# Kernel tuning notes

Hardware: AMD Instinct MI355X
Metric: run time of the kernel (lower is better)

The kernel has to match this reference:

```python
import jax, jax.numpy as jnp
import numpy as np
import math

N, E, D, H, L = 50000, 800000, 256, 8, 8
DK = D // H
DFF = 4 * D


def _layernorm(h, g, b, eps=1e-5):
    m = jnp.mean(h, axis=-1, keepdims=True)
    v = jnp.mean((h - m) ** 2, axis=-1, keepdims=True)
    return (h - m) * jax.lax.rsqrt(v + eps) * g + b


def setup_inputs() -> dict:
    key = jax.random.key(0)
    ks = jax.random.split(key, 16)
    s = 1.0 / math.sqrt(D)
    x = jax.random.normal(ks[0], (N, D), dtype=jnp.float32)
    # every node gets >=1 in-edge so z > 0 everywhere (as in real connected graphs)
    edge_src = jax.random.randint(ks[1], (E,), 0, N, dtype=jnp.int32)
    edge_dst = jnp.concatenate([
        jnp.arange(N, dtype=jnp.int32),
        jax.random.randint(ks[2], (E - N,), 0, N, dtype=jnp.int32),
    ])
    return {
        "x": x,
        "edge_src": edge_src,
        "edge_dst": edge_dst,
        "Wq": jax.random.normal(ks[3], (L, D, D), dtype=jnp.float32) * s,
        "bq": jnp.zeros((L, D), dtype=jnp.float32),
        "Wk": jax.random.normal(ks[4], (L, D, D), dtype=jnp.float32) * s,
        "Wv": jax.random.normal(ks[5], (L, D, D), dtype=jnp.float32) * s,
        "Wo": jax.random.normal(ks[6], (L, D, D), dtype=jnp.float32) * s,
        "bo": jnp.zeros((L, D), dtype=jnp.float32),
        "ln1_g": jnp.ones((L, D), dtype=jnp.float32),
        "ln1_b": jnp.zeros((L, D), dtype=jnp.float32),
        "W1": jax.random.normal(ks[7], (L, D, DFF), dtype=jnp.float32) * s,
        "b1": jnp.zeros((L, DFF), dtype=jnp.float32),
        "W2": jax.random.normal(ks[8], (L, DFF, D), dtype=jnp.float32) * (1.0 / math.sqrt(DFF)),
        "b2": jnp.zeros((L, D), dtype=jnp.float32),
        "ln2_g": jnp.ones((L, D), dtype=jnp.float32),
        "ln2_b": jnp.zeros((L, D), dtype=jnp.float32),
    }


def _layer(x, src, dst, Wq, bq, Wk, Wv, Wo, bo, g1, b1n, W1, b1, W2, b2, g2, b2n):
    n = x.shape[0]
    q = (x @ Wq + bq).reshape(n, H, DK)
    k = (x @ Wk).reshape(n, H, DK)
    v = (x @ Wv).reshape(n, H, DK)
    # edge score: src_dot_dst('k','q') -> [E, H]
    score = jnp.einsum('ehd,ehd->eh', k[src], q[dst])
    # scaled_exp: exp(clamp(score / sqrt(d_k), -5, 5))
    score = jnp.exp(jnp.clip(score / math.sqrt(DK), -5.0, 5.0))
    # u_mul_e + sum aggregation -> wv [N, H, DK]; copy_edge + sum -> z [N, H]
    msg = v[src] * score[:, :, None]
    wv = jax.ops.segment_sum(msg, dst, num_segments=n)
    z = jax.ops.segment_sum(score, dst, num_segments=n)
    o = (wv / z[:, :, None]).reshape(n, D)
    h = _layernorm(x + o @ Wo + bo, g1, b1n)
    # FFN with residual + layernorm
    ff = jax.nn.relu(h @ W1 + b1) @ W2 + b2
    return _layernorm(h + ff, g2, b2n)


def reference(x, edge_src, edge_dst, Wq, bq, Wk, Wv, Wo, bo, ln1_g, ln1_b,
              W1, b1, W2, b2, ln2_g, ln2_b):
    for i in range(L):
        x = _layer(x, edge_src, edge_dst, Wq[i], bq[i], Wk[i], Wv[i], Wo[i],
                   bo[i], ln1_g[i], ln1_b[i], W1[i], b1[i], W2[i], b2[i],
                   ln2_g[i], ln2_b[i])
    return x
```

## Files before the change

### kernel.cpp

```cpp
#include <hip/hip_runtime.h>
#include <cstdint>
#include <cstddef>

#define D 256
#define H 8
#define DFF 1024

typedef short s16x8 __attribute__((ext_vector_type(8)));
typedef float f32x4 __attribute__((ext_vector_type(4)));

static inline int cdiv(int a, int b) { return (a + b - 1) / b; }

__device__ inline uint16_t f2bf(float x) {
    unsigned u = __float_as_uint(x);
    u += 0x7FFFu + ((u >> 16) & 1u);
    return (uint16_t)(u >> 16);
}
__device__ inline float bf2f(uint16_t h) {
    return __uint_as_float(((unsigned)h) << 16);
}

__device__ inline void gload_lds16(const void* g, void* l) {
    __builtin_amdgcn_global_load_lds(
        (const __attribute__((address_space(1))) void*)g,
        (__attribute__((address_space(3))) void*)l, 16, 0, 0);
}

__device__ inline void vmcnt0() { asm volatile("s_waitcnt vmcnt(0)" ::: "memory"); }
__device__ inline void vmcnt3() { asm volatile("s_waitcnt vmcnt(3)" ::: "memory"); }
__device__ inline void vmcnt4() { asm volatile("s_waitcnt vmcnt(4)" ::: "memory"); }
__device__ inline void vmcnt5() { asm volatile("s_waitcnt vmcnt(5)" ::: "memory"); }
__device__ inline void lgkm0()  { asm volatile("s_waitcnt lgkmcnt(0)" ::: "memory"); }
#define SB0() __builtin_amdgcn_sched_barrier(0)
#define BARF() do { SB0(); __builtin_amdgcn_s_barrier(); SB0(); } while (0)

__global__ __launch_bounds__(256) void zero_int_kernel(int* __restrict__ p, int count)
{
    int i = blockIdx.x * blockDim.x + threadIdx.x;
    if (i < count) p[i] = 0;
}

__global__ __launch_bounds__(256) void count_deg_kernel(
    const int* __restrict__ edst, int* __restrict__ deg, int E)
{
    int e = blockIdx.x * blockDim.x + threadIdx.x;
    if (e < E) atomicAdd(&deg[edst[e]], 1);
}

__global__ __launch_bounds__(256) void block_sum_kernel(
    const int* __restrict__ deg, int* __restrict__ bsum, int N)
{
    int t = threadIdx.x;
    int gid = blockIdx.x * 256 + t;
    int val = (gid < N) ? deg[gid] : 0;
    #pragma unroll
    for (int o = 1; o < 64; o <<= 1) val += __shfl_xor(val, o);
    __shared__ int r[4];
    if ((t & 63) == 0) r[t >> 6] = val;
    __syncthreads();
    if (t == 0) bsum[blockIdx.x] = r[0] + r[1] + r[2] + r[3];
}

__global__ __launch_bounds__(256) void scan_bsum_kernel(int* __restrict__ bsum, int nb)
{
    __shared__ int tmp[256];
    int t = threadIdx.x;
    int val = (t < nb) ? bsum[t] : 0;
    tmp[t] = val;
    __syncthreads();
    for (int off = 1; off < 256; off <<= 1) {
        int add = (t >= off) ? tmp[t - off] : 0;
        __syncthreads();
        tmp[t] += add;
        __syncthreads();
    }
    if (t < nb) bsum[t] = tmp[t] - val;
}

__global__ __launch_bounds__(256) void scan_write_kernel(
    const int* __restrict__ deg, const int* __restrict__ bsum,
    int* __restrict__ rowptr, int* __restrict__ cursor, int N)
{
    __shared__ int tmp[256];
    int t = threadIdx.x;
    int gid = blockIdx.x * 256 + t;
    int val = (gid < N) ? deg[gid] : 0;
    tmp[t] = val;
    __syncthreads();
    for (int off = 1; off < 256; off <<= 1) {
        int add = (t >= off) ? tmp[t - off] : 0;
        __syncthreads();
        tmp[t] += add;
        __syncthreads();
    }
    int excl = tmp[t] - val + bsum[blockIdx.x];
    if (gid < N) { rowptr[gid] = excl; cursor[gid] = excl; }
    if (gid == N - 1) rowptr[N] = excl + val;
}

__global__ __launch_bounds__(256) void fill_csr_kernel(
    const int* __restrict__ esrc, const int* __restrict__ edst,
    int* __restrict__ cursor, int* __restrict__ csr_src, int E)
{
    int e = blockIdx.x * blockDim.x + threadIdx.x;
    if (e < E) {
        int pos = atomicAdd(&cursor[edst[e]], 1);
        csr_src[pos] = esrc[e];
    }
}

__global__ __launch_bounds__(256) void transpose_cast_kernel(
    const float* __restrict__ in, uint16_t* __restrict__ out,
    int R, int C, size_t inLS, size_t outLS)
{
    __shared__ float t[32][33];
    in  += blockIdx.z * inLS;
    out += blockIdx.z * outLS;
    int c0 = blockIdx.x * 32, r0 = blockIdx.y * 32;
    int tx = threadIdx.x, ty = threadIdx.y;
    #pragma unroll
    for (int i = 0; i < 4; ++i)
        t[ty + i * 8][tx] = in[(size_t)(r0 + ty + i * 8) * C + c0 + tx];
    __syncthreads();
    #pragma unroll
    for (int i = 0; i < 4; ++i)
        out[(size_t)(c0 + ty + i * 8) * R + r0 + tx] = f2bf(t[tx][ty + i * 8]);
}

__global__ __launch_bounds__(256) void cast_f32_bf16_kernel(
    const float* __restrict__ in, uint16_t* __restrict__ out, int n4)
{
    int i = blockIdx.x * blockDim.x + threadIdx.x;
    if (i >= n4) return;
    float4 f = ((const float4*)in)[i];
    uint16_t o0 = f2bf(f.x), o1 = f2bf(f.y), o2 = f2bf(f.z), o3 = f2bf(f.w);
    uint2 pk;
    pk.x = (unsigned)o0 | ((unsigned)o1 << 16);
    pk.y = (unsigned)o2 | ((unsigned)o3 << 16);
    ((uint2*)out)[i] = pk;
}

__global__ __launch_bounds__(256) void build_qkv_bias_kernel(
    const float* __restrict__ bq, float* __restrict__ qb, int total)
{
    int i = blockIdx.x * blockDim.x + threadIdx.x;
    if (i >= total) return;
    int l = i / 768, c = i - l * 768;
    qb[i] = (c < 256) ? bq[l * 256 + c] : 0.f;
}

__global__ __launch_bounds__(256) void gemm_bf16_kernel(
    const uint16_t* __restrict__ A, int lda, int M, int K,
    const uint16_t* __restrict__ BT, int Nc,
    const float* __restrict__ bias,
    uint16_t* __restrict__ Cb, int relu)
{
    __shared__ __align__(16) uint16_t As[2][128 * 32];
    __shared__ __align__(16) uint16_t Bs[2][128 * 32];

    const int tid  = threadIdx.x;
    const int lane = tid & 63;
    const int w    = tid >> 6;
    const int wr   = w >> 1, wc = w & 1;
    const int quad = lane >> 4;
    const int l15  = lane & 15;

    const int nwg = gridDim.x * gridDim.y;
    const int lin = blockIdx.y * gridDim.x + blockIdx.x;
    const int xcd = lin & 7, idx = lin >> 3;
    const int q8 = nwg >> 3, r8 = nwg & 7;
    const int lin2 = (xcd < r8 ? xcd * (q8 + 1) : r8 * (q8 + 1) + (xcd - r8) * q8) + idx;
    const int mt = lin2 % gridDim.x;
    const int nt = lin2 / gridDim.x;

    const int m0 = mt * 128;
    const int n0 = nt * 128;

    f32x4 acc[4][4] = {};

    const int jbase = w * 2;
    const int srow  = lane >> 2;
    const int skc   = (lane & 3) * 8;

    auto stage = [&](int b, int k0) {
        #pragma unroll
        for (int jj = 0; jj < 2; ++jj) {
            int j = jbase + jj;
            int r = j * 16 + srow;
            int gr = m0 + r; if (gr > M - 1) gr = M - 1;
            gload_lds16(A  + (size_t)gr * lda + k0 + skc, &As[b][j * 512]);
            gload_lds16(BT + (size_t)(n0 + r) * K + k0 + skc, &Bs[b][j * 512]);
        }
    };

    const int nsteps = K >> 5;
    stage(0, 0);
    for (int s = 0; s < nsteps; ++s) {
        if (s + 1 < nsteps) { stage((s + 1) & 1, (s + 1) << 5); vmcnt4(); }
        else vmcnt0();
        BARF();
        const int b = s & 1;
        s16x8 af[4], bf[4];
        #pragma unroll
        for (int t = 0; t < 4; ++t) {
            af[t] = *(const s16x8*)&As[b][(wr * 64 + t * 16 + l15) * 32 + quad * 8];
            bf[t] = *(const s16x8*)&Bs[b][(wc * 64 + t * 16 + l15) * 32 + quad * 8];
        }
        #pragma unroll
        for (int i = 0; i < 4; ++i)
            #pragma unroll
            for (int jt = 0; jt < 4; ++jt)
                acc[i][jt] = __builtin_amdgcn_mfma_f32_16x16x32_bf16(
                    af[i], bf[jt], acc[i][jt], 0, 0, 0);
        BARF();
    }

    float bv[4];
    #pragma unroll
    for (int jt = 0; jt < 4; ++jt)
        bv[jt] = bias ? bias[n0 + wc * 64 + jt * 16 + l15] : 0.f;

    #pragma unroll
    for (int i = 0; i < 4; ++i) {
        #pragma unroll
        for (int r = 0; r < 4; ++r) {
            int m = m0 + wr * 64 + i * 16 + quad * 4 + r;
            if (m >= M) continue;
            #pragma unroll
            for (int jt = 0; jt < 4; ++jt) {
                int n = n0 + wc * 64 + jt * 16 + l15;
                float val = acc[i][jt][r] + bv[jt];
                if (relu) val = fmaxf(val, 0.f);
                Cb[(size_t)m * Nc + n] = f2bf(val);
            }
        }
    }
}

__global__ __launch_bounds__(256) void gemm_ln_kernel(
    const uint16_t* __restrict__ A, int lda, int M, int K,
    const uint16_t* __restrict__ BT,
    const float* __restrict__ bias,
    const float* __restrict__ resid,
    const float* __restrict__ g, const float* __restrict__ b,
    float* __restrict__ Cf, uint16_t* __restrict__ Cb)
{
    __shared__ __align__(16) uint16_t As[2][64 * 32];
    __shared__ __align__(16) uint16_t Bs[2][256 * 32];
    __shared__ float sS[64][4];
    __shared__ float sQ[64][4];

    const int tid  = threadIdx.x;
    const int lane = tid & 63;
    const int w    = tid >> 6;
    const int quad = lane >> 4;
    const int l15  = lane & 15;

    const int m0 = blockIdx.x * 64;

    f32x4 acc[4][4] = {};

    auto stage = [&](int bb, int k0) {
        {
            int r = tid >> 2, kc = (tid & 3) * 8;
            int gr = m0 + r; if (gr > M - 1) gr = M - 1;
            gload_lds16(A + (size_t)gr * lda + k0 + kc, &As[bb][tid * 8]);
        }
        #pragma unroll
        for (int i = 0; i < 4; ++i) {
            int slot = i * 256 + tid;
            int n = slot >> 2, kc = (slot & 3) * 8;
            gload_lds16(BT + (size_t)n * K + k0 + kc, &Bs[bb][slot * 8]);
        }
    };

    const int nsteps = K >> 5;
    stage(0, 0);
    for (int s = 0; s < nsteps; ++s) {
        if (s + 1 < nsteps) { stage((s + 1) & 1, (s + 1) << 5); vmcnt5(); }
        else vmcnt0();
        BARF();
        const int bb = s & 1;
        s16x8 af[4], bf[4];
        #pragma unroll
        for (int t = 0; t < 4; ++t) {
            af[t] = *(const s16x8*)&As[bb][(t * 16 + l15) * 32 + quad * 8];
            bf[t] = *(const s16x8*)&Bs[bb][(w * 64 + t * 16 + l15) * 32 + quad * 8];
        }
        #pragma unroll
        for (int i = 0; i < 4; ++i)
            #pragma unroll
            for (int jt = 0; jt < 4; ++jt)
                acc[i][jt] = __builtin_amdgcn_mfma_f32_16x16x32_bf16(
                    af[i], bf[jt], acc[i][jt], 0, 0, 0);
        BARF();
    }

    float bv[4], gv[4], bbv[4];
    #pragma unroll
    for (int jt = 0; jt < 4; ++jt) {
        int n = w * 64 + jt * 16 + l15;
        bv[jt]  = bias[n];
        gv[jt]  = g[n];
        bbv[jt] = b[n];
    }

    #pragma unroll
    for (int i = 0; i < 4; ++i) {
        #pragma unroll
        for (int r = 0; r < 4; ++r) {
            int ml = i * 16 + quad * 4 + r;
            int m  = m0 + ml;
            bool valid = (m < M);
            float s = 0.f, s2 = 0.f;
            #pragma unroll
            for (int jt = 0; jt < 4; ++jt) {
                int n = w * 64 + jt * 16 + l15;
                float val = acc[i][jt][r] + bv[jt];
                if (valid) val += resid[(size_t)m * 256 + n];
                acc[i][jt][r] = val;
                s += val;
                s2 += val * val;
            }
            #pragma unroll
            for (int o = 1; o < 16; o <<= 1) {
                s  += __shfl_xor(s, o);
                s2 += __shfl_xor(s2, o);
            }
            if (l15 == 0) { sS[ml][w] = s; sQ[ml][w] = s2; }
        }
    }
    __syncthreads();

    #pragma unroll
    for (int i = 0; i < 4; ++i) {
        #pragma unroll
        for (int r = 0; r < 4; ++r) {
            int ml = i * 16 + quad * 4 + r;
            int m  = m0 + ml;
            if (m >= M) continue;
            float s  = sS[ml][0] + sS[ml][1] + sS[ml][2] + sS[ml][3];
            float s2 = sQ[ml][0] + sQ[ml][1] + sQ[ml][2] + sQ[ml][3];
            float mean = s * (1.f / 256.f);
            float var  = s2 * (1.f / 256.f) - mean * mean;
            float rstd = rsqrtf(var + 1e-5f);
            #pragma unroll
            for (int jt = 0; jt < 4; ++jt) {
                int n = w * 64 + jt * 16 + l15;
                float out = (acc[i][jt][r] - mean) * rstd * gv[jt] + bbv[jt];
                Cf[(size_t)m * 256 + n] = out;
                if (Cb) Cb[(size_t)m * 256 + n] = f2bf(out);
            }
        }
    }
}

__global__ __launch_bounds__(256) void ffn_fused_kernel(
    const uint16_t* __restrict__ A,
    int M,
    const uint16_t* __restrict__ BT1,
    const float* __restrict__ b1,
    const uint16_t* __restrict__ BT2,
    const float* __restrict__ b2,
    const float* __restrict__ resid,
    const float* __restrict__ g, const float* __restrict__ b,
    float* __restrict__ Cf, uint16_t* __restrict__ Cb)
{
    __shared__ __align__(16) uint16_t U[2][8192];
    __shared__ __align__(16) uint16_t Ts[4][64][40];

    const int tid  = threadIdx.x;
    const int lane = tid & 63;
    const int w    = tid >> 6;
    const int quad = lane >> 4;
    const int l15  = lane & 15;
    const int m0   = blockIdx.x * 64;

    f32x4 acc2[4][4] = {};

    auto stage1 = [&](int bb, int c, int k0) {
        {
            int r = tid >> 2, kc = (tid & 3) * 8;
            int gr = m0 + r; if (gr > M - 1) gr = M - 1;
            gload_lds16(A + (size_t)gr * 256 + k0 + kc, &U[bb][tid * 8]);
        }
        #pragma unroll
        for (int i = 0; i < 2; ++i) {
            int slot = i * 256 + tid;
            int n = slot >> 2, kc = (slot & 3) * 8;
            gload_lds16(BT1 + (size_t)(c * 128 + n) * 256 + k0 + kc,
                        &U[bb][2048 + slot * 8]);
        }
    };
    auto stage2 = [&](int bb, int c, int ts) {
        #pragma unroll
        for (int i = 0; i < 4; ++i) {
            int slot = i * 256 + tid;
            int n = slot >> 2, kc = (slot & 3) * 8;
            gload_lds16(BT2 + (size_t)n * 1024 + c * 128 + ts * 32 + kc,
                        &U[bb][slot * 8]);
        }
    };

    for (int c = 0; c < 8; ++c) {
        f32x4 acc1[4][2] = {};

        stage1(0, c, 0);
        for (int ks = 0; ks < 8; ++ks) {
            if (ks < 7) { stage1((ks + 1) & 1, c, (ks + 1) << 5); vmcnt3(); }
            else vmcnt0();
            BARF();
            const int bb = ks & 1;
            s16x8 af[4], bf1[2];
            #pragma unroll
            for (int t = 0; t < 4; ++t)
                af[t] = *(const s16x8*)&U[bb][(t * 16 + l15) * 32 + quad * 8];
            #pragma unroll
            for (int jt = 0; jt < 2; ++jt)
                bf1[jt] = *(const s16x8*)&U[bb][2048 + (w * 32 + jt * 16 + l15) * 32 + quad * 8];
            #pragma unroll
            for (int i = 0; i < 4; ++i)
                #pragma unroll
                for (int jt = 0; jt < 2; ++jt)
                    acc1[i][jt] = __builtin_amdgcn_mfma_f32_16x16x32_bf16(
                        af[i], bf1[jt], acc1[i][jt], 0, 0, 0);
            BARF();
        }

        float bv1[2];
        #pragma unroll
        for (int jt = 0; jt < 2; ++jt)
            bv1[jt] = b1[c * 128 + w * 32 + jt * 16 + l15];
        #pragma unroll
        for (int i = 0; i < 4; ++i)
            #pragma unroll
            for (int r = 0; r < 4; ++r) {
                int ml = i * 16 + quad * 4 + r;
                #pragma unroll
                for (int jt = 0; jt < 2; ++jt) {
                    float val = acc1[i][jt][r] + bv1[jt];
                    val = fmaxf(val, 0.f);
                    Ts[w][ml][jt * 16 + l15] = f2bf(val);
                }
            }
        lgkm0();
        BARF();

        stage2(0, c, 0);
        for (int ts = 0; ts < 4; ++ts) {
            if (ts < 3) { stage2((ts + 1) & 1, c, ts + 1); vmcnt4(); }
            else vmcnt0();
            BARF();
            const int bb = ts & 1;
            s16x8 af2[4], bf2[4];
            #pragma unroll
            for (int i = 0; i < 4; ++i)
                af2[i] = *(const s16x8*)&Ts[ts][i * 16 + l15][quad * 8];
            #pragma unroll
            for (int jt = 0; jt < 4; ++jt)
                bf2[jt] = *(const s16x8*)&U[bb][(w * 64 + jt * 16 + l15) * 32 + quad * 8];
            #pragma unroll
            for (int i = 0; i < 4; ++i)
                #pragma unroll
                for (int jt = 0; jt < 4; ++jt)
                    acc2[i][jt] = __builtin_amdgcn_mfma_f32_16x16x32_bf16(
                        af2[i], bf2[jt], acc2[i][jt], 0, 0, 0);
            BARF();
        }
    }

    float* sS = (float*)&U[0][0];
    float* sQ = (float*)&U[0][512];

    float bv[4], gv[4], bbv[4];
    #pragma unroll
    for (int jt = 0; jt < 4; ++jt) {
        int n = w * 64 + jt * 16 + l15;
        bv[jt]  = b2[n];
        gv[jt]  = g[n];
        bbv[jt] = b[n];
    }

    #pragma unroll
    for (int i = 0; i < 4; ++i) {
        #pragma unroll
        for (int r = 0; r < 4; ++r) {
            int ml = i * 16 + quad * 4 + r;
            int m  = m0 + ml;
            bool valid = (m < M);
            float s = 0.f, s2 = 0.f;
            #pragma unroll
            for (int jt = 0; jt < 4; ++jt) {
                float val = acc2[i][jt][r] + bv[jt];
                if (valid) val += resid[(size_t)m * 256 + w * 64 + jt * 16 + l15];
                acc2[i][jt][r] = val;
                s += val;
                s2 += val * val;
            }
            #pragma unroll
            for (int o = 1; o < 16; o <<= 1) {
                s  += __shfl_xor(s, o);
                s2 += __shfl_xor(s2, o);
            }
            if (l15 == 0) { sS[ml * 4 + w] = s; sQ[ml * 4 + w] = s2; }
        }
    }
    __syncthreads();

    #pragma unroll
    for (int i = 0; i < 4; ++i) {
        #pragma unroll
        for (int r = 0; r < 4; ++r) {
            int ml = i * 16 + quad * 4 + r;
            int m  = m0 + ml;
            if (m >= M) continue;
            float s  = sS[ml * 4 + 0] + sS[ml * 4 + 1] + sS[ml * 4 + 2] + sS[ml * 4 + 3];
            float s2 = sQ[ml * 4 + 0] + sQ[ml * 4 + 1] + sQ[ml * 4 + 2] + sQ[ml * 4 + 3];
            float mean = s * (1.f / 256.f);
            float var  = s2 * (1.f / 256.f) - mean * mean;
            float rstd = rsqrtf(var + 1e-5f);
            #pragma unroll
            for (int jt = 0; jt < 4; ++jt) {
                int n = w * 64 + jt * 16 + l15;
                float out = (acc2[i][jt][r] - mean) * rstd * gv[jt] + bbv[jt];
                Cf[(size_t)m * 256 + n] = out;
                if (Cb) Cb[(size_t)m * 256 + n] = f2bf(out);
            }
        }
    }
}

__global__ __launch_bounds__(256) void node_attn_kernel(
    uint16_t* __restrict__ qkv,
    const int* __restrict__ rowptr, const int* __restrict__ csr_src, int N)
{
    int node = (blockIdx.x * blockDim.x + threadIdx.x) >> 6;
    int lane = threadIdx.x & 63;
    if (node >= N) return;

    uint16_t* qp = qkv + (size_t)node * 768 + lane * 4;
    uint2 qu = *(const uint2*)qp;
    float q0 = bf2f((uint16_t)(qu.x & 0xFFFF)), q1 = bf2f((uint16_t)(qu.x >> 16));
    float q2 = bf2f((uint16_t)(qu.y & 0xFFFF)), q3 = bf2f((uint16_t)(qu.y >> 16));

    float a0 = 0.f, a1 = 0.f, a2 = 0.f, a3 = 0.f, zacc = 0.f;
    const float inv_sqrt_dk = 0.17677669529663687f;

    int beg = rowptr[node], end = rowptr[node + 1];
    int i = beg;
    for (; i + 1 < end; i += 2) {
        int s0 = csr_src[i], s1 = csr_src[i + 1];
        const uint16_t* b0 = qkv + (size_t)s0 * 768;
        const uint16_t* b1 = qkv + (size_t)s1 * 768;
        uint2 ku0 = *(const uint2*)(b0 + 256 + lane * 4);
        uint2 ku1 = *(const uint2*)(b1 + 256 + lane * 4);
        uint2 vu0 = *(const uint2*)(b0 + 512 + lane * 4);
        uint2 vu1 = *(const uint2*)(b1 + 512 + lane * 4);

        float p0 = bf2f((uint16_t)(ku0.x & 0xFFFF)) * q0
                 + bf2f((uint16_t)(ku0.x >> 16))   * q1
                 + bf2f((uint16_t)(ku0.y & 0xFFFF)) * q2
                 + bf2f((uint16_t)(ku0.y >> 16))   * q3;
        float p1 = bf2f((uint16_t)(ku1.x & 0xFFFF)) * q0
                 + bf2f((uint16_t)(ku1.x >> 16))   * q1
                 + bf2f((uint16_t)(ku1.y & 0xFFFF)) * q2
                 + bf2f((uint16_t)(ku1.y >> 16))   * q3;
        p0 += __shfl_xor(p0, 1); p1 += __shfl_xor(p1, 1);
        p0 += __shfl_xor(p0, 2); p1 += __shfl_xor(p1, 2);
        p0 += __shfl_xor(p0, 4); p1 += __shfl_xor(p1, 4);
        float sc0 = __expf(fminf(fmaxf(p0 * inv_sqrt_dk, -5.f), 5.f));
        float sc1 = __expf(fminf(fmaxf(p1 * inv_sqrt_dk, -5.f), 5.f));

        a0 += bf2f((uint16_t)(vu0.x & 0xFFFF)) * sc0;
        a1 += bf2f((uint16_t)(vu0.x >> 16))   * sc0;
        a2 += bf2f((uint16_t)(vu0.y & 0xFFFF)) * sc0;
        a3 += bf2f((uint16_t)(vu0.y >> 16))   * sc0;
        zacc += sc0;
        a0 += bf2f((uint16_t)(vu1.x & 0xFFFF)) * sc1;
        a1 += bf2f((uint16_t)(vu1.x >> 16))   * sc1;
        a2 += bf2f((uint16_t)(vu1.y & 0xFFFF)) * sc1;
        a3 += bf2f((uint16_t)(vu1.y >> 16))   * sc1;
        zacc += sc1;
    }
    if (i < end) {
        int s = csr_src[i];
        const uint16_t* base = qkv + (size_t)s * 768;
        uint2 ku = *(const uint2*)(base + 256 + lane * 4);
        float p = bf2f((uint16_t)(ku.x & 0xFFFF)) * q0
                + bf2f((uint16_t)(ku.x >> 16))   * q1
                + bf2f((uint16_t)(ku.y & 0xFFFF)) * q2
                + bf2f((uint16_t)(ku.y >> 16))   * q3;
        p += __shfl_xor(p, 1);
        p += __shfl_xor(p, 2);
        p += __shfl_xor(p, 4);
        float sc = __expf(fminf(fmaxf(p * inv_sqrt_dk, -5.f), 5.f));
        uint2 vu = *(const uint2*)(base + 512 + lane * 4);
        a0 += bf2f((uint16_t)(vu.x & 0xFFFF)) * sc;
        a1 += bf2f((uint16_t)(vu.x >> 16))   * sc;
        a2 += bf2f((uint16_t)(vu.y & 0xFFFF)) * sc;
        a3 += bf2f((uint16_t)(vu.y >> 16))   * sc;
        zacc += sc;
    }
    float inv = 1.f / zacc;
    uint2 pk;
    pk.x = (unsigned)f2bf(a0 * inv) | ((unsigned)f2bf(a1 * inv) << 16);
    pk.y = (unsigned)f2bf(a2 * inv) | ((unsigned)f2bf(a3 * inv) << 16);
    *(uint2*)qp = pk;
}

extern "C" void kernel_launch(void* const* d_in, const int* in_sizes, int n_in,
                              void* d_out, int out_size, void* d_ws, size_t ws_size,
                              hipStream_t stream)
{
    const float* x0   = (const float*)d_in[0];
    const int* esrc   = (const int*)d_in[1];
    const int* edst   = (const int*)d_in[2];
    const float* Wq   = (const float*)d_in[3];
    const float* bq   = (const float*)d_in[4];
    const float* Wk   = (const float*)d_in[5];
    const float* Wv   = (const float*)d_in[6];
    const float* Wo   = (const float*)d_in[7];
    const float* bo   = (const float*)d_in[8];
    const float* ln1g = (const float*)d_in[9];
    const float* ln1b = (const float*)d_in[10];
    const float* W1   = (const float*)d_in[11];
    const float* b1   = (const float*)d_in[12];
    const float* W2   = (const float*)d_in[13];
    const float* b2   = (const float*)d_in[14];
    const float* ln2g = (const float*)d_in[15];
    const float* ln2b = (const float*)d_in[16];

    const int N = in_sizes[0] / D;
    const int E = in_sizes[1];
    const int L = in_sizes[3] / (D * D);
    const size_t ND = (size_t)N * D;

    char* p = (char*)d_ws;
    float* bufX = (float*)p;         p += ND * 4;
    uint16_t* xb  = (uint16_t*)p;    p += ND * 2;
    uint16_t* qkv = (uint16_t*)p;    p += (size_t)N * 768 * 2;
    uint16_t* hb  = (uint16_t*)p;    p += ND * 2;
    uint16_t* BTqkv = (uint16_t*)p;  p += (size_t)L * 768 * 256 * 2;
    uint16_t* BTo   = (uint16_t*)p;  p += (size_t)L * 256 * 256 * 2;
    uint16_t* BT1   = (uint16_t*)p;  p += (size_t)L * 1024 * 256 * 2;
    uint16_t* BT2   = (uint16_t*)p;  p += (size_t)L * 256 * 1024 * 2;
    float* qbias    = (float*)p;     p += (size_t)L * 768 * 4;
    int* rowptr  = (int*)p;          p += (size_t)(N + 1) * 4;
    int* cursor  = (int*)p;          p += (size_t)N * 4;
    int* deg     = cursor;
    int* csr_src = (int*)p;          p += (size_t)E * 4;
    int* bsum    = (int*)p;

    const int nb = cdiv(N, 256);
    dim3 blk(256);
    int edgeBlocks = cdiv(E, 256);
    int nodeBlocks = cdiv(N, 4);

    dim3 tb(32, 8);
    transpose_cast_kernel<<<dim3(8, 8, L), tb, 0, stream>>>(Wq, BTqkv, 256, 256, (size_t)65536, (size_t)768 * 256);
    transpose_cast_kernel<<<dim3(8, 8, L), tb, 0, stream>>>(Wk, BTqkv + 256 * 256, 256, 256, (size_t)65536, (size_t)768 * 256);
    transpose_cast_kernel<<<dim3(8, 8, L), tb, 0, stream>>>(Wv, BTqkv + 512 * 256, 256, 256, (size_t)65536, (size_t)768 * 256);
    transpose_cast_kernel<<<dim3(8, 8, L), tb, 0, stream>>>(Wo, BTo, 256, 256, (size_t)65536, (size_t)65536);
    transpose_cast_kernel<<<dim3(32, 8, L), tb, 0, stream>>>(W1, BT1, 256, 1024, (size_t)262144, (size_t)262144);
    transpose_cast_kernel<<<dim3(8, 32, L), tb, 0, stream>>>(W2, BT2, 1024, 256, (size_t)262144, (size_t)262144);
    build_qkv_bias_kernel<<<cdiv(L * 768, 256), blk, 0, stream>>>(bq, qbias, L * 768);
    cast_f32_bf16_kernel<<<cdiv((int)(ND / 4), 256), blk, 0, stream>>>(x0, xb, (int)(ND / 4));

    zero_int_kernel<<<cdiv(N, 256), blk, 0, stream>>>(deg, N);
    count_deg_kernel<<<edgeBlocks, blk, 0, stream>>>(edst, deg, E);
    block_sum_kernel<<<nb, blk, 0, stream>>>(deg, bsum, N);
    scan_bsum_kernel<<<1, blk, 0, stream>>>(bsum, nb);
    scan_write_kernel<<<nb, blk, 0, stream>>>(deg, bsum, rowptr, cursor, N);
    fill_csr_kernel<<<edgeBlocks, blk, 0, stream>>>(esrc, edst, cursor, csr_src, E);

    const int Mt128 = cdiv(N, 128);
    const int Mt64  = cdiv(N, 64);
    dim3 gQKV(Mt128, 768 / 128);
    dim3 gLN(Mt64, 1);

    for (int l = 0; l < L; ++l) {
        const uint16_t* BTqkv_l = BTqkv + (size_t)l * 768 * 256;
        const uint16_t* BTo_l   = BTo + (size_t)l * 65536;
        const uint16_t* BT1_l   = BT1 + (size_t)l * 262144;
        const uint16_t* BT2_l   = BT2 + (size_t)l * 262144;
        const float* xin_f = (l == 0) ? x0 : bufX;

        gemm_bf16_kernel<<<gQKV, blk, 0, stream>>>(xb, 256, N, 256, BTqkv_l, 768,
            qbias + (size_t)l * 768, qkv, 0);

        node_attn_kernel<<<nodeBlocks, blk, 0, stream>>>(qkv, rowptr, csr_src, N);

        gemm_ln_kernel<<<gLN, blk, 0, stream>>>(qkv, 768, N, 256, BTo_l,
            bo + (size_t)l * 256, xin_f, ln1g + (size_t)l * 256, ln1b + (size_t)l * 256,
            bufX, hb);

        float* fout = (l == L - 1) ? (float*)d_out : bufX;
        ffn_fused_kernel<<<gLN, blk, 0, stream>>>(hb, N, BT1_l,
            b1 + (size_t)l * 1024, BT2_l, b2 + (size_t)l * 256, bufX,
            ln2g + (size_t)l * 256, ln2b + (size_t)l * 256,
            fout, (l == L - 1) ? nullptr : xb);

        xin_f = bufX;
    }
}
```

Before: 3.131 ms.

## Triple-buffer FFN kernel loads across stages and swizzle hidden tile LDS

Replaces the per-stage double-buffered loads in the fused FFN kernel with a single unified 96-step load sequence over three LDS buffers. Loads stay two steps ahead across the boundary between the first and second GEMM and across chunks, so the pipeline no longer drains at each stage start. The intermediate ReLU tile drops its padding in favour of an XOR swizzle meant to avoid bank conflicts. This costs more LDS per block, which may reduce occupancy, and relies on precise vmcnt counts.

```diff
diff --git a/kernel.cpp b/kernel.cpp
--- a/kernel.cpp
+++ b/kernel.cpp
@@ -27,9 +27,9 @@
 }
 
 __device__ inline void vmcnt0() { asm volatile("s_waitcnt vmcnt(0)" ::: "memory"); }
-__device__ inline void vmcnt3() { asm volatile("s_waitcnt vmcnt(3)" ::: "memory"); }
 __device__ inline void vmcnt4() { asm volatile("s_waitcnt vmcnt(4)" ::: "memory"); }
 __device__ inline void vmcnt5() { asm volatile("s_waitcnt vmcnt(5)" ::: "memory"); }
+__device__ inline void vmcnt6() { asm volatile("s_waitcnt vmcnt(6)" ::: "memory"); }
 __device__ inline void lgkm0()  { asm volatile("s_waitcnt lgkmcnt(0)" ::: "memory"); }
 #define SB0() __builtin_amdgcn_sched_barrier(0)
 #define BARF() do { SB0(); __builtin_amdgcn_s_barrier(); SB0(); } while (0)
@@ -366,8 +366,8 @@
     const float* __restrict__ g, const float* __restrict__ b,
     float* __restrict__ Cf, uint16_t* __restrict__ Cb)
 {
-    __shared__ __align__(16) uint16_t U[2][8192];
-    __shared__ __align__(16) uint16_t Ts[4][64][40];
+    __shared__ __align__(16) uint16_t U[3][8192];
+    __shared__ __align__(16) uint16_t Ts[4][64][32];
 
     const int tid  = threadIdx.x;
     const int lane = tid & 63;
@@ -378,46 +378,57 @@
 
     f32x4 acc2[4][4] = {};
 
-    auto stage1 = [&](int bb, int c, int k0) {
-        {
-            int r = tid >> 2, kc = (tid & 3) * 8;
-            int gr = m0 + r; if (gr > M - 1) gr = M - 1;
-            gload_lds16(A + (size_t)gr * 256 + k0 + kc, &U[bb][tid * 8]);
-        }
-        #pragma unroll
-        for (int i = 0; i < 2; ++i) {
-            int slot = i * 256 + tid;
-            int n = slot >> 2, kc = (slot & 3) * 8;
-            gload_lds16(BT1 + (size_t)(c * 128 + n) * 256 + k0 + kc,
-                        &U[bb][2048 + slot * 8]);
+    auto issue = [&](int q) {
+        if (q >= 96) return;
+        const int slot = q % 3;
+        const int qc = q / 12;
+        const int r  = q - qc * 12;
+        if (r < 8) {
+            const int k0 = r << 5;
+            {
+                int rr = tid >> 2, kc = (tid & 3) * 8;
+                int gr = m0 + rr; if (gr > M - 1) gr = M - 1;
+                gload_lds16(A + (size_t)gr * 256 + k0 + kc, &U[slot][tid * 8]);
+            }
+            #pragma unroll
+            for (int i = 0; i < 2; ++i) {
+                int s2 = i * 256 + tid;
+                int n = s2 >> 2, kc = (s2 & 3) * 8;
+                gload_lds16(BT1 + (size_t)(qc * 128 + n) * 256 + k0 + kc,
+                            &U[slot][2048 + s2 * 8]);
+            }
+        } else {
+            const int ts = r - 8;
+            #pragma unroll
+            for (int i = 0; i < 4; ++i) {
+                int s2 = i * 256 + tid;
+                int n = s2 >> 2, kc = (s2 & 3) * 8;
+                gload_lds16(BT2 + (size_t)n * 1024 + qc * 128 + ts * 32 + kc,
+                            &U[slot][s2 * 8]);
+            }
         }
     };
-    auto stage2 = [&](int bb, int c, int ts) {
-        #pragma unroll
-        for (int i = 0; i < 4; ++i) {
-            int slot = i * 256 + tid;
-            int n = slot >> 2, kc = (slot & 3) * 8;
-            gload_lds16(BT2 + (size_t)n * 1024 + c * 128 + ts * 32 + kc,
-                        &U[bb][slot * 8]);
-        }
-    };
+
+    issue(0);
+    issue(1);
 
     for (int c = 0; c < 8; ++c) {
         f32x4 acc1[4][2] = {};
-
-        stage1(0, c, 0);
+        const int pbase = c * 12;
+
         for (int ks = 0; ks < 8; ++ks) {
-            if (ks < 7) { stage1((ks + 1) & 1, c, (ks + 1) << 5); vmcnt3(); }
-            else vmcnt0();
+            const int p = pbase + ks;
+            issue(p + 2);
+            vmcnt6();
             BARF();
-            const int bb = ks & 1;
+            const uint16_t* Us = U[p % 3];
             s16x8 af[4], bf1[2];
             #pragma unroll
             for (int t = 0; t < 4; ++t)
-                af[t] = *(const s16x8*)&U[bb][(t * 16 + l15) * 32 + quad * 8];
+                af[t] = *(const s16x8*)&Us[(t * 16 + l15) * 32 + quad * 8];
             #pragma unroll
             for (int jt = 0; jt < 2; ++jt)
-                bf1[jt] = *(const s16x8*)&U[bb][2048 + (w * 32 + jt * 16 + l15) * 32 + quad * 8];
+                bf1[jt] = *(const s16x8*)&Us[2048 + (w * 32 + jt * 16 + l15) * 32 + quad * 8];
             #pragma unroll
             for (int i = 0; i < 4; ++i)
                 #pragma unroll
@@ -431,34 +442,43 @@
         #pragma unroll
         for (int jt = 0; jt < 2; ++jt)
             bv1[jt] = b1[c * 128 + w * 32 + jt * 16 + l15];
-        #pragma unroll
-        for (int i = 0; i < 4; ++i)
-            #pragma unroll
-            for (int r = 0; r < 4; ++r) {
-                int ml = i * 16 + quad * 4 + r;
+        {
+            uint16_t* tsw = &Ts[w][0][0];
+            #pragma unroll
+            for (int i = 0; i < 4; ++i)
                 #pragma unroll
-                for (int jt = 0; jt < 2; ++jt) {
-                    float val = acc1[i][jt][r] + bv1[jt];
-                    val = fmaxf(val, 0.f);
-                    Ts[w][ml][jt * 16 + l15] = f2bf(val);
+                for (int r = 0; r < 4; ++r) {
+                    int ml = i * 16 + quad * 4 + r;
+                    int sw = ((ml >> 1) & 3) << 3;
+                    #pragma unroll
+                    for (int jt = 0; jt < 2; ++jt) {
+                        float val = acc1[i][jt][r] + bv1[jt];
+                        val = fmaxf(val, 0.f);
+                        tsw[(ml * 32 + jt * 16 + l15) ^ sw] = f2bf(val);
+                    }
                 }
-            }
+        }
         lgkm0();
         BARF();
 
-        stage2(0, c, 0);
         for (int ts = 0; ts < 4; ++ts) {
-            if (ts < 3) { stage2((ts + 1) & 1, c, ts + 1); vmcnt4(); }
-            else vmcnt0();
+            const int p = pbase + 8 + ts;
+            issue(p + 2);
+            if (c == 7 && ts == 2) vmcnt4();
+            else if (c == 7 && ts == 3) vmcnt0();
+            else vmcnt6();
             BARF();
-            const int bb = ts & 1;
+            const uint16_t* Us = U[p % 3];
+            const uint16_t* tsr = &Ts[ts][0][0];
             s16x8 af2[4], bf2[4];
             #pragma unroll
-            for (int i = 0; i < 4; ++i)
-                af2[i] = *(const s16x8*)&Ts[ts][i * 16 + l15][quad * 8];
+            for (int i = 0; i < 4; ++i) {
+                int row = i * 16 + l15;
+                af2[i] = *(const s16x8*)&tsr[(row * 32 + quad * 8) ^ (((row >> 1) & 3) << 3)];
+            }
             #pragma unroll
             for (int jt = 0; jt < 4; ++jt)
-                bf2[jt] = *(const s16x8*)&U[bb][(w * 64 + jt * 16 + l15) * 32 + quad * 8];
+                bf2[jt] = *(const s16x8*)&Us[(w * 64 + jt * 16 + l15) * 32 + quad * 8];
             #pragma unroll
             for (int i = 0; i < 4; ++i)
                 #pragma unroll
```

After: 3.901 ms. 1.25x slower.
